# Optimization experiments

Measured on AMD Instinct MI355X. Metric: run time of the kernel, lower is better.

Reference implementation:

```python
import jax, jax.numpy as jnp
import numpy as np

N_NODES = 100000
N_EDGES = 600000
NFEAT = 128
HIDDEN = 64
NCLASS = 40


def _sage_conv(x, edge_index, Wl, bl, Wr):
    """PyG SAGEConv with mean aggregation.

    out = lin_l(mean_{j in N(i)} x_j) + lin_r(x_i)
    edge_index[0] = source j, edge_index[1] = target i.
    """
    src, dst = edge_index[0], edge_index[1]
    n = x.shape[0]
    # scatter-mean: sum messages then divide by in-degree (0-degree -> 0)
    msg_sum = jax.ops.segment_sum(x[src], dst, num_segments=n)          # [N, F]
    deg = jax.ops.segment_sum(jnp.ones_like(src, dtype=x.dtype), dst,
                              num_segments=n)                            # [N]
    agg = msg_sum / jnp.maximum(deg, 1.0)[:, None]
    return agg @ Wl + bl + x @ Wr


def setup_inputs() -> dict:
    key = jax.random.key(0)
    ks = jax.random.split(key, 8)
    x = jax.random.normal(ks[0], (N_NODES, NFEAT), dtype=jnp.float32)
    edge_index = jax.random.randint(ks[1], (2, N_EDGES), 0, N_NODES, dtype=jnp.int64)
    s1 = 1.0 / np.sqrt(NFEAT)
    s2 = 1.0 / np.sqrt(HIDDEN)
    return {
        "x": x,
        "edge_index": edge_index,
        "W1l": jax.random.uniform(ks[2], (NFEAT, HIDDEN), jnp.float32, -s1, s1),
        "b1": jnp.zeros((HIDDEN,), jnp.float32),
        "W1r": jax.random.uniform(ks[3], (NFEAT, HIDDEN), jnp.float32, -s1, s1),
        "W2l": jax.random.uniform(ks[4], (HIDDEN, NCLASS), jnp.float32, -s2, s2),
        "b2": jnp.zeros((NCLASS,), jnp.float32),
        "W2r": jax.random.uniform(ks[5], (HIDDEN, NCLASS), jnp.float32, -s2, s2),
    }


def reference(x, edge_index, W1l, b1, W1r, W2l, b2, W2r):
    h = _sage_conv(x, edge_index, W1l, b1, W1r)   # [N, 64]
    h = jax.nn.sigmoid(h)
    out = _sage_conv(h, edge_index, W2l, b2, W2r)  # [N, nclass]
    return out
```

## Files before the change

kernel.cpp:

```cpp
#include <hip/hip_runtime.h>
#include <hip/hip_bf16.h>


#define N_FEAT 128
#define HID 64
#define NCLS 40
#define NE_BLK 4096
#define ECAP 1024

typedef short short8 __attribute__((ext_vector_type(8)));
typedef float floatx4 __attribute__((ext_vector_type(4)));

static __device__ __forceinline__ short f2bf(float x) {
    __hip_bfloat16 h = __float2bfloat16(x);
    return __builtin_bit_cast(short, h);
}
static __device__ __forceinline__ float bf2f(unsigned short u) {
    unsigned int v = ((unsigned int)u) << 16;
    return __builtin_bit_cast(float, v);
}

#define GATHER4(SRC, Zsrc, AC)                                               \
    for (int r = 0; r < d; r += 4) {                                         \
        int i1 = (r + 1 < d) ? r + 1 : d - 1;                                \
        int i2 = (r + 2 < d) ? r + 2 : d - 1;                                \
        int i3 = (r + 3 < d) ? r + 3 : d - 1;                                \
        int j0 = SRC[s + r], j1 = SRC[s + i1];                               \
        int j2 = SRC[s + i2], j3 = SRC[s + i3];                              \
        uint2 v0 = *(const uint2*)(Zsrc + (size_t)j0 * 64 + col * 4);        \
        uint2 v1 = *(const uint2*)(Zsrc + (size_t)j1 * 64 + col * 4);        \
        uint2 v2 = *(const uint2*)(Zsrc + (size_t)j2 * 64 + col * 4);        \
        uint2 v3 = *(const uint2*)(Zsrc + (size_t)j3 * 64 + col * 4);        \
        float w1 = (r + 1 < d) ? 1.f : 0.f;                                  \
        float w2 = (r + 2 < d) ? 1.f : 0.f;                                  \
        float w3 = (r + 3 < d) ? 1.f : 0.f;                                  \
        AC[0] += bf2f((unsigned short)(v0.x & 0xffffu));                     \
        AC[1] += bf2f((unsigned short)(v0.x >> 16));                         \
        AC[2] += bf2f((unsigned short)(v0.y & 0xffffu));                     \
        AC[3] += bf2f((unsigned short)(v0.y >> 16));                         \
        AC[0] = fmaf(w1, bf2f((unsigned short)(v1.x & 0xffffu)), AC[0]);     \
        AC[1] = fmaf(w1, bf2f((unsigned short)(v1.x >> 16)), AC[1]);         \
        AC[2] = fmaf(w1, bf2f((unsigned short)(v1.y & 0xffffu)), AC[2]);     \
        AC[3] = fmaf(w1, bf2f((unsigned short)(v1.y >> 16)), AC[3]);         \
        AC[0] = fmaf(w2, bf2f((unsigned short)(v2.x & 0xffffu)), AC[0]);     \
        AC[1] = fmaf(w2, bf2f((unsigned short)(v2.x >> 16)), AC[1]);         \
        AC[2] = fmaf(w2, bf2f((unsigned short)(v2.y & 0xffffu)), AC[2]);     \
        AC[3] = fmaf(w2, bf2f((unsigned short)(v2.y >> 16)), AC[3]);         \
        AC[0] = fmaf(w3, bf2f((unsigned short)(v3.x & 0xffffu)), AC[0]);     \
        AC[1] = fmaf(w3, bf2f((unsigned short)(v3.x >> 16)), AC[1]);         \
        AC[2] = fmaf(w3, bf2f((unsigned short)(v3.y & 0xffffu)), AC[2]);     \
        AC[3] = fmaf(w3, bf2f((unsigned short)(v3.y >> 16)), AC[3]);         \
    }

#define TILE_SORT()                                                          \
    __syncthreads();     \
    if (t < 64) cnt[t] = 0;                                                  \
    __syncthreads();                                                         \
    for (int j = t; j < cn; j += 256)                                        \
        atomicAdd(&cnt[ebuf[E0 + c0 + j] >> 26], 1);                         \
    __syncthreads();                                                         \
    if (t == 0) {                                                            \
        int run = 0;                                                         \
        for (int i = 0; i < 64; ++i) { pos[i] = run; run += cnt[i]; }        \
    }                                                                        \
    __syncthreads();                                                         \
    for (int j = t; j < cn; j += 256) {                                      \
        unsigned u = ebuf[E0 + c0 + j];                                      \
        int r = atomicAdd(&pos[u >> 26], 1);                                 \
        elist[r] = (int)(u & 0x03FFFFFFu);                                   \
    }                                                                        \
    __syncthreads();

__global__ void prep_hist(const float* __restrict__ W1l, const float* __restrict__ W1r,
                          const float* __restrict__ W2l, const float* __restrict__ W2r,
                          unsigned short* __restrict__ wt1,
                          unsigned short* __restrict__ wt2,
                          int* __restrict__ flags,
                          const int* __restrict__ ei, int ne, int n,
                          int* __restrict__ bh, int nbe) {
    __shared__ int bins[2048];
    const int b = blockIdx.x, t = threadIdx.x;
    const int nbuck = (n + 63) >> 6;
    for (int i = t; i < nbuck; i += 256) bins[i] = 0;
    __syncthreads();
    const int e0 = b * NE_BLK;
    const int lim = (e0 + NE_BLK < ne) ? (e0 + NE_BLK) : ne;
    for (int e = e0 + t; e < lim; e += 256)
        atomicAdd(&bins[ei[ne + e] >> 6], 1);

    int i = b * 256 + t;
    if (i < 128 * 128) {
        int nn = i >> 7, k = i & 127;
        float v = (nn < 64) ? W1l[k * 64 + nn] : W1r[k * 64 + (nn - 64)];
        wt1[nn * 128 + k] = (unsigned short)f2bf(v);
    } else if (i < 128 * 128 + 48 * 128) {
        int j = i - 128 * 128;
        int nn = j >> 7, k = j & 127;
        float v = 0.f;
        if (nn < 40)
            v = (k < 64) ? W2l[k * 40 + nn] : W2r[(k - 64) * 40 + nn];
        wt2[nn * 128 + k] = (unsigned short)f2bf(v);
    }
    if (i < 256) flags[i] = 0;

    __syncthreads();
    for (int j = t; j < nbuck; j += 256) bh[(size_t)j * nbe + b] = bins[j];
}

__global__ void scan_fused(const int* __restrict__ in, int* __restrict__ pre,
                           int m, int* __restrict__ bsums,
                           int* __restrict__ flags) {
    __shared__ int lds[256];
    __shared__ int look[128];
    __shared__ int sprefix;
    const int b = blockIdx.x, t = threadIdx.x;
    const int base = b * 2048 + t * 8;
    int v[8], s = 0;
#pragma unroll
    for (int i = 0; i < 8; ++i) {
        int idx = base + i;
        v[i] = (idx < m) ? in[idx] : 0;
        s += v[i];
    }
    lds[t] = s;
    __syncthreads();
    for (int o = 1; o < 256; o <<= 1) {
        int y = (t >= o) ? lds[t - o] : 0;
        __syncthreads();
        lds[t] += y;
        __syncthreads();
    }
    if (t == 255) {
        __hip_atomic_store(&bsums[b], lds[255], __ATOMIC_RELEASE,
                           __HIP_MEMORY_SCOPE_AGENT);
        __hip_atomic_store(&flags[b], 1, __ATOMIC_RELEASE,
                           __HIP_MEMORY_SCOPE_AGENT);
    }
    if (t < 128) look[t] = 0;
    __syncthreads();
    if (t < b) {
        while (__hip_atomic_load(&flags[t], __ATOMIC_ACQUIRE,
                                 __HIP_MEMORY_SCOPE_AGENT) == 0) {}
        look[t] = __hip_atomic_load(&bsums[t], __ATOMIC_RELAXED,
                                    __HIP_MEMORY_SCOPE_AGENT);
    }
    __syncthreads();
    if (t == 0) {
        int p = 0;
        for (int i = 0; i < b; ++i) p += look[i];
        sprefix = p;
    }
    __syncthreads();
    int run = ((t == 0) ? 0 : lds[t - 1]) + sprefix;
#pragma unroll
    for (int i = 0; i < 8; ++i) {
        run += v[i];
        int idx = base + i;
        if (idx < m) pre[idx + 1] = run;
    }
    if (b == 0 && t == 0) pre[0] = 0;
}

static __device__ __forceinline__ void gemm1_body(
    short* __restrict__ smem, const float* __restrict__ x,
    const unsigned short* __restrict__ Wt, unsigned short* __restrict__ Zl,
    unsigned short* __restrict__ Zr, int n, int bid) {
    constexpr int K = 128, LDA = K + 8, M = 128, MT = 8, KS = 4, QROW = 16;
    short* At = smem;
    short* Bt = smem + 64 * LDA;
    const int t = threadIdx.x;
    const int nodeBase = bid * 64;

    for (int q = t; q < 64 * QROW; q += 256) {
        int row = q / QROW;
        int k0 = (q % QROW) * 8;
        int node = nodeBase + row;
        short8 s = {0, 0, 0, 0, 0, 0, 0, 0};
        if (node < n) {
            const float* A = x + (size_t)node * K + k0;
            float4 v0 = *(const float4*)A;
            float4 v1 = *(const float4*)(A + 4);
            s[0] = f2bf(v0.x); s[1] = f2bf(v0.y);
            s[2] = f2bf(v0.z); s[3] = f2bf(v0.w);
            s[4] = f2bf(v1.x); s[5] = f2bf(v1.y);
            s[6] = f2bf(v1.z); s[7] = f2bf(v1.w);
        }
        *(short8*)&At[row * LDA + k0] = s;
    }
    for (int q = t; q < M * QROW; q += 256) {
        int row = q / QROW;
        int k0 = (q % QROW) * 8;
        *(short8*)&Bt[row * LDA + k0] =
            *(const short8*)((const short*)Wt + (size_t)row * K + k0);
    }
    __syncthreads();

    const int wave = t >> 6;
    const int lane = t & 63;
    const int m0 = wave * 16;
    const int fl = lane & 15;
    const int quad = lane >> 4;

    floatx4 acc[MT];
#pragma unroll
    for (int nt = 0; nt < MT; ++nt) acc[nt] = (floatx4){0.f, 0.f, 0.f, 0.f};

#pragma unroll
    for (int ks = 0; ks < KS; ++ks) {
        const int kb = ks * 32 + quad * 8;
        short8 a = *(const short8*)&At[(m0 + fl) * LDA + kb];
#pragma unroll
        for (int nt = 0; nt < MT; ++nt) {
            short8 b = *(const short8*)&Bt[(nt * 16 + fl) * LDA + kb];
            acc[nt] = __builtin_amdgcn_mfma_f32_16x16x32_bf16(a, b, acc[nt], 0, 0, 0);
        }
    }

#pragma unroll
    for (int nt = 0; nt < MT; ++nt) {
        const int col = nt * 16 + fl;
#pragma unroll
        for (int r = 0; r < 4; ++r) {
            int node = nodeBase + m0 + quad * 4 + r;
            if (node < n) {
                unsigned short v = (unsigned short)f2bf(acc[nt][r]);
                if (col < HID)
                    Zl[(size_t)node * HID + col] = v;
                else
                    Zr[(size_t)node * HID + (col - HID)] = v;
            }
        }
    }
}

__global__ __launch_bounds__(256) void scatter_gemm1(
    const int* __restrict__ ei, int ne, int n, const int* __restrict__ sbase,
    unsigned* __restrict__ ebuf, int nbe, const float* __restrict__ x,
    const unsigned short* __restrict__ wt1, unsigned short* __restrict__ zl,
    unsigned short* __restrict__ zr) {
    __shared__ __align__(16) short smem[(64 + 128) * 136];
    const int b = blockIdx.x;
    if (b < nbe) {
        int* bins = (int*)smem;
        const int t = threadIdx.x;
        const int nbuck = (n + 63) >> 6;
        for (int i = t; i < nbuck; i += 256) bins[i] = 0;
        __syncthreads();
        const int e0 = b * NE_BLK;
        const int lim = (e0 + NE_BLK < ne) ? (e0 + NE_BLK) : ne;
        for (int e = e0 + t; e < lim; e += 256) {
            int d = ei[ne + e];
            int s = ei[e];
            int bk = d >> 6;
            int r = atomicAdd(&bins[bk], 1);
            int p = sbase[(size_t)bk * nbe + b] + r;
            ebuf[p] = ((unsigned)(d & 63) << 26) | (unsigned)s;
        }
    } else {
        gemm1_body(smem, x, wt1, zl, zr, n, b - nbe);
    }
}

__global__ __launch_bounds__(256) void agg_h(
    const unsigned short* __restrict__ Zl, const unsigned short* __restrict__ Zr,
    const unsigned* __restrict__ ebuf, const int* __restrict__ sbase, int nbe,
    const float* __restrict__ bias, unsigned short* __restrict__ hout, int n) {
    __shared__ int elist[ECAP];
    __shared__ int cnt[64];
    __shared__ int pos[64];
    const int t = threadIdx.x;
    const int tile = blockIdx.x;
    const int base = tile * 64;
    const int E0 = sbase[(size_t)tile * nbe];
    const int E1 = sbase[(size_t)(tile + 1) * nbe];
    const int nedge = E1 - E0;

    const int lane = t & 63, wave = t >> 6;
    const int sub = lane >> 4, col = lane & 15;

    float a[4][4];
    int totd[4];
#pragma unroll
    for (int p = 0; p < 4; ++p) {
        totd[p] = 0;
#pragma unroll
        for (int j = 0; j < 4; ++j) a[p][j] = 0.f;
    }

    for (int c0 = 0; c0 < nedge; c0 += ECAP) {
        const int cn = (nedge - c0 < ECAP) ? (nedge - c0) : ECAP;
        TILE_SORT()
#pragma unroll
        for (int p = 0; p < 4; ++p) {
            const int i = wave * 16 + p * 4 + sub;
            const int s = pos[i] - cnt[i];
            const int d = cnt[i];
            totd[p] += d;
            float* AC = a[p];
            GATHER4(elist, Zl, AC)
        }
    }

#pragma unroll
    for (int p = 0; p < 4; ++p) {
        const int i = wave * 16 + p * 4 + sub;
        const int node = base + i;
        if (node < n) {
            float inv = 1.0f / fmaxf((float)totd[p], 1.0f);
            uint2 z = *(const uint2*)(Zr + (size_t)node * 64 + col * 4);
            float4 bb = ((const float4*)bias)[col];
            float r0 = a[p][0] * inv + bf2f((unsigned short)(z.x & 0xffffu)) + bb.x;
            float r1 = a[p][1] * inv + bf2f((unsigned short)(z.x >> 16)) + bb.y;
            float r2 = a[p][2] * inv + bf2f((unsigned short)(z.y & 0xffffu)) + bb.z;
            float r3 = a[p][3] * inv + bf2f((unsigned short)(z.y >> 16)) + bb.w;
            r0 = 1.0f / (1.0f + __expf(-r0));
            r1 = 1.0f / (1.0f + __expf(-r1));
            r2 = 1.0f / (1.0f + __expf(-r2));
            r3 = 1.0f / (1.0f + __expf(-r3));
            uint2 pk;
            pk.x = (unsigned)(unsigned short)f2bf(r0) |
                   ((unsigned)(unsigned short)f2bf(r1) << 16);
            pk.y = (unsigned)(unsigned short)f2bf(r2) |
                   ((unsigned)(unsigned short)f2bf(r3) << 16);
            *(uint2*)(hout + (size_t)node * 64 + col * 4) = pk;
        }
    }
}

__global__ __launch_bounds__(256) void agg_gemm2(
    const unsigned short* __restrict__ h, const unsigned short* __restrict__ Wt,
    const float* __restrict__ bias, const unsigned* __restrict__ ebuf,
    const int* __restrict__ sbase, int nbe, float* __restrict__ out, int n) {
    constexpr int LDA = 136;
    __shared__ __align__(16) short At[64 * LDA];
    __shared__ __align__(16) short Bt[48 * LDA];
    __shared__ int elist[ECAP];
    __shared__ int cnt[64];
    __shared__ int pos[64];
    const int t = threadIdx.x;
    const int tile = blockIdx.x;
    const int base = tile * 64;
    const int E0 = sbase[(size_t)tile * nbe];
    const int E1 = sbase[(size_t)(tile + 1) * nbe];
    const int nedge = E1 - E0;

    for (int q = t; q < 64 * 8; q += 256) {
        int row = q >> 3, k0 = (q & 7) * 8;
        int node = base + row;
        short8 s = {0, 0, 0, 0, 0, 0, 0, 0};
        if (node < n) s = *(const short8*)(h + (size_t)node * 64 + k0);
        *(short8*)&At[row * LDA + 64 + k0] = s;
    }
    for (int q = t; q < 48 * 16; q += 256) {
        int row = q >> 4, k0 = (q & 15) * 8;
        *(short8*)&Bt[row * LDA + k0] =
            *(const short8*)((const short*)Wt + (size_t)row * 128 + k0);
    }

    const int lane = t & 63, wave = t >> 6;
    const int sub = lane >> 4, col = lane & 15;

    float a[4][4];
    int totd[4];
#pragma unroll
    for (int p = 0; p < 4; ++p) {
        totd[p] = 0;
#pragma unroll
        for (int j = 0; j < 4; ++j) a[p][j] = 0.f;
    }

    for (int c0 = 0; c0 < nedge; c0 += ECAP) {
        const int cn = (nedge - c0 < ECAP) ? (nedge - c0) : ECAP;
        TILE_SORT()
#pragma unroll
        for (int p = 0; p < 4; ++p) {
            const int i = wave * 16 + p * 4 + sub;
            const int s = pos[i] - cnt[i];
            const int d = cnt[i];
            totd[p] += d;
            float* AC = a[p];
            GATHER4(elist, h, AC)
        }
    }

#pragma unroll
    for (int p = 0; p < 4; ++p) {
        const int i = wave * 16 + p * 4 + sub;
        float inv = 1.0f / fmaxf((float)totd[p], 1.0f);
        uint2 pk;
        pk.x = (unsigned)(unsigned short)f2bf(a[p][0] * inv) |
               ((unsigned)(unsigned short)f2bf(a[p][1] * inv) << 16);
        pk.y = (unsigned)(unsigned short)f2bf(a[p][2] * inv) |
               ((unsigned)(unsigned short)f2bf(a[p][3] * inv) << 16);
        *(uint2*)&At[i * LDA + col * 4] = pk;
    }
    __syncthreads();

    const int m0 = wave * 16;
    const int fl = lane & 15;
    const int quad = lane >> 4;
    floatx4 acc[3];
#pragma unroll
    for (int nt = 0; nt < 3; ++nt) acc[nt] = (floatx4){0.f, 0.f, 0.f, 0.f};
#pragma unroll
    for (int ks = 0; ks < 4; ++ks) {
        const int kb = ks * 32 + quad * 8;
        short8 av = *(const short8*)&At[(m0 + fl) * LDA + kb];
#pragma unroll
        for (int nt = 0; nt < 3; ++nt) {
            short8 bv = *(const short8*)&Bt[(nt * 16 + fl) * LDA + kb];
            acc[nt] = __builtin_amdgcn_mfma_f32_16x16x32_bf16(av, bv, acc[nt], 0, 0, 0);
        }
    }
#pragma unroll
    for (int nt = 0; nt < 3; ++nt) {
        const int col2 = nt * 16 + fl;
        if (col2 < NCLS) {
            float bv = bias[col2];
#pragma unroll
            for (int r = 0; r < 4; ++r) {
                int node = base + m0 + quad * 4 + r;
                if (node < n)
                    out[(size_t)node * NCLS + col2] = acc[nt][r] + bv;
            }
        }
    }
}

extern "C" void kernel_launch(void* const* d_in, const int* in_sizes, int n_in,
                              void* d_out, int out_size, void* d_ws,
                              size_t ws_size, hipStream_t stream) {
    const float* x = (const float*)d_in[0];
    const int* ei = (const int*)d_in[1];
    const float* W1l = (const float*)d_in[2];
    const float* b1 = (const float*)d_in[3];
    const float* W1r = (const float*)d_in[4];
    const float* W2l = (const float*)d_in[5];
    const float* b2 = (const float*)d_in[6];
    const float* W2r = (const float*)d_in[7];
    float* out = (float*)d_out;

    const int n = in_sizes[0] / N_FEAT;
    const int ne = in_sizes[1] / 2;

    const int nbe = (ne + NE_BLK - 1) / NE_BLK;
    const int nbuck = (n + 63) >> 6;
    const int tot = nbuck * nbe;

    unsigned short* zl1 = (unsigned short*)d_ws;
    unsigned short* zr1 = zl1 + (size_t)n * HID;
    unsigned short* h = zr1 + (size_t)n * HID;
    unsigned short* wt1 = h + (size_t)n * HID;
    unsigned short* wt2 = wt1 + 128 * 128;
    unsigned* ebuf = (unsigned*)(wt2 + 48 * 128);
    int* bh = (int*)(ebuf + ne);
    int* sbase = bh + tot;
    int* bsums = sbase + (tot + 1);
    int* flags = bsums + 256;

    const int gblocks = (n + 63) / 64;
    const int nsb = (tot + 2047) / 2048;

    prep_hist<<<nbe, 256, 0, stream>>>(W1l, W1r, W2l, W2r, wt1, wt2, flags,
                                       ei, ne, n, bh, nbe);
    scan_fused<<<nsb, 256, 0, stream>>>(bh, sbase, tot, bsums, flags);
    scatter_gemm1<<<nbe + gblocks, 256, 0, stream>>>(ei, ne, n, sbase, ebuf,
                                                     nbe, x, wt1, zl1, zr1);
    agg_h<<<gblocks, 256, 0, stream>>>(zl1, zr1, ebuf, sbase, nbe, b1, h, n);
    agg_gemm2<<<gblocks, 256, 0, stream>>>(h, wt2, b2, ebuf, sbase, nbe, out, n);
}
```

Baseline: 186.3 us.

## Fuse scan into scatter/GEMM1 kernel and reuse sorted CSR in second aggregation

Folds the decoupled-lookback scan into the scatter+GEMM1 launch: scan blocks run first and signal a global flag, and scatter blocks spin on that flag before they start. This removes one kernel launch. agg_h now writes the per-tile sorted edge list and the node degrees, so agg_gemm2 can load them directly instead of redoing the tile sort. Other changes are a larger ECAP and a wave-shuffle prefix scan replacing the serial one. The spin-wait relies on the scan blocks being scheduled ahead of the waiting scatter blocks, and the extra csr/deg writes and reads add memory traffic.

New measurement: 239.1 us. 1.28x slower.

```diff
diff --git a/kernel.cpp b/kernel.cpp
--- a/kernel.cpp
+++ b/kernel.cpp
@@ -6,7 +6,7 @@
 #define HID 64
 #define NCLS 40
 #define NE_BLK 4096
-#define ECAP 1024
+#define ECAP 2048
 
 typedef short short8 __attribute__((ext_vector_type(8)));
 typedef float floatx4 __attribute__((ext_vector_type(4)));
@@ -53,15 +53,21 @@
     }
 
 #define TILE_SORT()                                                          \
-    __syncthreads();     \
+    __syncthreads();                                                         \
     if (t < 64) cnt[t] = 0;                                                  \
     __syncthreads();                                                         \
     for (int j = t; j < cn; j += 256)                                        \
         atomicAdd(&cnt[ebuf[E0 + c0 + j] >> 26], 1);                         \
     __syncthreads();                                                         \
-    if (t == 0) {                                                            \
-        int run = 0;                                                         \
-        for (int i = 0; i < 64; ++i) { pos[i] = run; run += cnt[i]; }        \
+    if (t < 64) {                                                            \
+        int v = cnt[t];                                                      \
+        int xx = v;                                                          \
+        _Pragma("unroll")                                                    \
+        for (int o = 1; o < 64; o <<= 1) {                                   \
+            int y = __shfl_up(xx, o);                                        \
+            if (t >= o) xx += y;                                             \
+        }                                                                    \
+        pos[t] = xx - v;                       \
     }                                                                        \
     __syncthreads();                                                         \
     for (int j = t; j < cn; j += 256) {                                      \
@@ -107,60 +113,6 @@
     for (int j = t; j < nbuck; j += 256) bh[(size_t)j * nbe + b] = bins[j];
 }
 
-__global__ void scan_fused(const int* __restrict__ in, int* __restrict__ pre,
-                           int m, int* __restrict__ bsums,
-                           int* __restrict__ flags) {
-    __shared__ int lds[256];
-    __shared__ int look[128];
-    __shared__ int sprefix;
-    const int b = blockIdx.x, t = threadIdx.x;
-    const int base = b * 2048 + t * 8;
-    int v[8], s = 0;
-#pragma unroll
-    for (int i = 0; i < 8; ++i) {
-        int idx = base + i;
-        v[i] = (idx < m) ? in[idx] : 0;
-        s += v[i];
-    }
-    lds[t] = s;
-    __syncthreads();
-    for (int o = 1; o < 256; o <<= 1) {
-        int y = (t >= o) ? lds[t - o] : 0;
-        __syncthreads();
-        lds[t] += y;
-        __syncthreads();
-    }
-    if (t == 255) {
-        __hip_atomic_store(&bsums[b], lds[255], __ATOMIC_RELEASE,
-                           __HIP_MEMORY_SCOPE_AGENT);
-        __hip_atomic_store(&flags[b], 1, __ATOMIC_RELEASE,
-                           __HIP_MEMORY_SCOPE_AGENT);
-    }
-    if (t < 128) look[t] = 0;
-    __syncthreads();
-    if (t < b) {
-        while (__hip_atomic_load(&flags[t], __ATOMIC_ACQUIRE,
-                                 __HIP_MEMORY_SCOPE_AGENT) == 0) {}
-        look[t] = __hip_atomic_load(&bsums[t], __ATOMIC_RELAXED,
-                                    __HIP_MEMORY_SCOPE_AGENT);
-    }
-    __syncthreads();
-    if (t == 0) {
-        int p = 0;
-        for (int i = 0; i < b; ++i) p += look[i];
-        sprefix = p;
-    }
-    __syncthreads();
-    int run = ((t == 0) ? 0 : lds[t - 1]) + sprefix;
-#pragma unroll
-    for (int i = 0; i < 8; ++i) {
-        run += v[i];
-        int idx = base + i;
-        if (idx < m) pre[idx + 1] = run;
-    }
-    if (b == 0 && t == 0) pre[0] = 0;
-}
-
 static __device__ __forceinline__ void gemm1_body(
     short* __restrict__ smem, const float* __restrict__ x,
     const unsigned short* __restrict__ Wt, unsigned short* __restrict__ Zl,
@@ -233,38 +185,108 @@
     }
 }
 
-__global__ __launch_bounds__(256) void scatter_gemm1(
-    const int* __restrict__ ei, int ne, int n, const int* __restrict__ sbase,
-    unsigned* __restrict__ ebuf, int nbe, const float* __restrict__ x,
+__global__ __launch_bounds__(256) void scan_scatter_gemm1(
+    const int* __restrict__ bh, int* __restrict__ sbase, int tot, int nsb,
+    int* __restrict__ bsums, int* __restrict__ flags,
+    const int* __restrict__ ei, int ne, int n, unsigned* __restrict__ ebuf,
+    int nbe, const float* __restrict__ x,
     const unsigned short* __restrict__ wt1, unsigned short* __restrict__ zl,
     unsigned short* __restrict__ zr) {
     __shared__ __align__(16) short smem[(64 + 128) * 136];
     const int b = blockIdx.x;
-    if (b < nbe) {
+    const int t = threadIdx.x;
+    if (b < nsb) {
+        int* lds = (int*)smem;
+        int* look = lds + 256;
+        int* sprefix = look + 128;
+        const int base = b * 2048 + t * 8;
+        int v[8], s = 0;
+#pragma unroll
+        for (int i = 0; i < 8; ++i) {
+            int idx = base + i;
+            v[i] = (idx < tot) ? bh[idx] : 0;
+            s += v[i];
+        }
+        lds[t] = s;
+        __syncthreads();
+        for (int o = 1; o < 256; o <<= 1) {
+            int y = (t >= o) ? lds[t - o] : 0;
+            __syncthreads();
+            lds[t] += y;
+            __syncthreads();
+        }
+        if (t == 255) {
+            __hip_atomic_store(&bsums[b], lds[255], __ATOMIC_RELEASE,
+                               __HIP_MEMORY_SCOPE_AGENT);
+            __hip_atomic_store(&flags[b], 1, __ATOMIC_RELEASE,
+                               __HIP_MEMORY_SCOPE_AGENT);
+        }
+        if (t < 128) look[t] = 0;
+        __syncthreads();
+        if (t < b) {
+            while (__hip_atomic_load(&flags[t], __ATOMIC_ACQUIRE,
+                                     __HIP_MEMORY_SCOPE_AGENT) == 0) {}
+            look[t] = __hip_atomic_load(&bsums[t], __ATOMIC_RELAXED,
+                                        __HIP_MEMORY_SCOPE_AGENT);
+        }
+        __syncthreads();
+        if (t == 0) {
+            int p = 0;
+            for (int i = 0; i < b; ++i) p += look[i];
+            sprefix[0] = p;
+        }
+        __syncthreads();
+        int run = ((t == 0) ? 0 : lds[t - 1]) + sprefix[0];
+#pragma unroll
+        for (int i = 0; i < 8; ++i) {
+            run += v[i];
+            int idx = base + i;
+            if (idx < tot) sbase[idx + 1] = run;
+        }
+        if (b == 0 && t == 0) sbase[0] = 0;
+        __threadfence();
+        __syncthreads();
+        if (t == 0) {
+            int arrived = __hip_atomic_fetch_add(&flags[129], 1,
+                                                 __ATOMIC_ACQ_REL,
+                                                 __HIP_MEMORY_SCOPE_AGENT);
+            if (arrived == nsb - 1)
+                __hip_atomic_store(&flags[128], 1, __ATOMIC_RELEASE,
+                                   __HIP_MEMORY_SCOPE_AGENT);
+        }
+    } else if (b < nsb + nbe) {
+        if (t == 0) {
+            while (__hip_atomic_load(&flags[128], __ATOMIC_ACQUIRE,
+                                     __HIP_MEMORY_SCOPE_AGENT) == 0) {}
+        }
+        __syncthreads();
+        (void)__hip_atomic_load(&flags[128], __ATOMIC_ACQUIRE,
+                                __HIP_MEMORY_SCOPE_AGENT);
         int* bins = (int*)smem;
-        const int t = threadIdx.x;
+        const int sb = b - nsb;
         const int nbuck = (n + 63) >> 6;
         for (int i = t; i < nbuck; i += 256) bins[i] = 0;
         __syncthreads();
-        const int e0 = b * NE_BLK;
+        const int e0 = sb * NE_BLK;
         const int lim = (e0 + NE_BLK < ne) ? (e0 + NE_BLK) : ne;
         for (int e = e0 + t; e < lim; e += 256) {
             int d = ei[ne + e];
             int s = ei[e];
             int bk = d >> 6;
             int r = atomicAdd(&bins[bk], 1);
-            int p = sbase[(size_t)bk * nbe + b] + r;
+            int p = sbase[(size_t)bk * nbe + sb] + r;
             ebuf[p] = ((unsigned)(d & 63) << 26) | (unsigned)s;
         }
     } else {
-        gemm1_body(smem, x, wt1, zl, zr, n, b - nbe);
+        gemm1_body(smem, x, wt1, zl, zr, n, b - nsb - nbe);
     }
 }
 
 __global__ __launch_bounds__(256) void agg_h(
     const unsigned short* __restrict__ Zl, const unsigned short* __restrict__ Zr,
     const unsigned* __restrict__ ebuf, const int* __restrict__ sbase, int nbe,
-    const float* __restrict__ bias, unsigned short* __restrict__ hout, int n) {
+    const float* __restrict__ bias, unsigned short* __restrict__ hout,
+    int* __restrict__ csrO, int* __restrict__ degO, int n) {
     __shared__ int elist[ECAP];
     __shared__ int cnt[64];
     __shared__ int pos[64];
@@ -290,6 +312,7 @@
     for (int c0 = 0; c0 < nedge; c0 += ECAP) {
         const int cn = (nedge - c0 < ECAP) ? (nedge - c0) : ECAP;
         TILE_SORT()
+        for (int j = t; j < cn; j += 256) csrO[E0 + c0 + j] = elist[j];
 #pragma unroll
         for (int p = 0; p < 4; ++p) {
             const int i = wave * 16 + p * 4 + sub;
@@ -306,6 +329,7 @@
         const int i = wave * 16 + p * 4 + sub;
         const int node = base + i;
         if (node < n) {
+            if (col == 0) degO[node] = totd[p];
             float inv = 1.0f / fmaxf((float)totd[p], 1.0f);
             uint2 z = *(const uint2*)(Zr + (size_t)node * 64 + col * 4);
             float4 bb = ((const float4*)bias)[col];
@@ -330,7 +354,8 @@
 __global__ __launch_bounds__(256) void agg_gemm2(
     const unsigned short* __restrict__ h, const unsigned short* __restrict__ Wt,
     const float* __restrict__ bias, const unsigned* __restrict__ ebuf,
-    const int* __restrict__ sbase, int nbe, float* __restrict__ out, int n) {
+    const int* __restrict__ sbase, int nbe, const int* __restrict__ csrI,
+    const int* __restrict__ degI, float* __restrict__ out, int n) {
     constexpr int LDA = 136;
     __shared__ __align__(16) short At[64 * LDA];
     __shared__ __align__(16) short Bt[48 * LDA];
@@ -369,17 +394,43 @@
         for (int j = 0; j < 4; ++j) a[p][j] = 0.f;
     }
 
-    for (int c0 = 0; c0 < nedge; c0 += ECAP) {
-        const int cn = (nedge - c0 < ECAP) ? (nedge - c0) : ECAP;
-        TILE_SORT()
+    if (nedge <= ECAP) {
+        for (int j = t; j < nedge; j += 256) elist[j] = csrI[E0 + j];
+        if (t < 64) {
+            int node = base + t;
+            int v = (node < n) ? degI[node] : 0;
+            cnt[t] = v;
+            int xx = v;
+#pragma unroll
+            for (int o = 1; o < 64; o <<= 1) {
+                int y = __shfl_up(xx, o);
+                if (t >= o) xx += y;
+            }
+            pos[t] = xx;
+        }
+        __syncthreads();
 #pragma unroll
         for (int p = 0; p < 4; ++p) {
             const int i = wave * 16 + p * 4 + sub;
             const int s = pos[i] - cnt[i];
             const int d = cnt[i];
-            totd[p] += d;
+            totd[p] = d;
             float* AC = a[p];
             GATHER4(elist, h, AC)
+        }
+    } else {
+        for (int c0 = 0; c0 < nedge; c0 += ECAP) {
+            const int cn = (nedge - c0 < ECAP) ? (nedge - c0) : ECAP;
+            TILE_SORT()
+#pragma unroll
+            for (int p = 0; p < 4; ++p) {
+                const int i = wave * 16 + p * 4 + sub;
+                const int s = pos[i] - cnt[i];
+                const int d = cnt[i];
+                totd[p] += d;
+                float* AC = a[p];
+                GATHER4(elist, h, AC)
+            }
         }
     }
 
@@ -453,7 +504,9 @@
     unsigned short* wt1 = h + (size_t)n * HID;
     unsigned short* wt2 = wt1 + 128 * 128;
     unsigned* ebuf = (unsigned*)(wt2 + 48 * 128);
-    int* bh = (int*)(ebuf + ne);
+    int* csr = (int*)(ebuf + ne);
+    int* deg = csr + ne;
+    int* bh = deg + n;
     int* sbase = bh + tot;
     int* bsums = sbase + (tot + 1);
     int* flags = bsums + 256;
@@ -463,9 +516,11 @@
 
     prep_hist<<<nbe, 256, 0, stream>>>(W1l, W1r, W2l, W2r, wt1, wt2, flags,
                                        ei, ne, n, bh, nbe);
-    scan_fused<<<nsb, 256, 0, stream>>>(bh, sbase, tot, bsums, flags);
-    scatter_gemm1<<<nbe + gblocks, 256, 0, stream>>>(ei, ne, n, sbase, ebuf,
-                                                     nbe, x, wt1, zl1, zr1);
-    agg_h<<<gblocks, 256, 0, stream>>>(zl1, zr1, ebuf, sbase, nbe, b1, h, n);
-    agg_gemm2<<<gblocks, 256, 0, stream>>>(h, wt2, b2, ebuf, sbase, nbe, out, n);
-}
+    scan_scatter_gemm1<<<nsb + nbe + gblocks, 256, 0, stream>>>(
+        bh, sbase, tot, nsb, bsums, flags, ei, ne, n, ebuf, nbe, x, wt1, zl1,
+        zr1);
+    agg_h<<<gblocks, 256, 0, stream>>>(zl1, zr1, ebuf, sbase, nbe, b1, h, csr,
+                                       deg, n);
+    agg_gemm2<<<gblocks, 256, 0, stream>>>(h, wt2, b2, ebuf, sbase, nbe, csr,
+                                           deg, out, n);
+}
```
